# Kernel tuning notes

Hardware: AMD Instinct MI355X
Metric: run time of the kernel (lower is better)

## Reference

```python
import jax, jax.numpy as jnp
import numpy as np

NQ = 8
NL = 6
DIM = 2 ** NQ
C64 = jnp.complex64
I2 = jnp.eye(2, dtype=C64)
PX = jnp.array([[0., 1.], [1., 0.]], dtype=C64)
PY = jnp.array([[0., -1j], [1j, 0.]], dtype=C64)
PZ = jnp.array([[1., 0.], [0., -1.]], dtype=C64)
# sign of Pauli-Z eigenvalue for each computational basis state, wires 0..3 (wire 0 = MSB)
_idx = np.arange(DIM)
_SIGNS = jnp.asarray(np.stack([1.0 - 2.0 * ((_idx >> (NQ - 1 - w)) & 1) for w in range(4)]).astype(np.float32))  # (4, 256)

def _rot(t, P):
    # exp(-i t/2 P) = cos(t/2) I - i sin(t/2) P
    th = t.astype(jnp.float32) / 2
    return jnp.cos(th) * I2 - 1j * jnp.sin(th) * P

def _apply1(st, U, w):
    # apply 2x2 unitary U on wire w; st: (B, 2,2,...,2)
    s = jnp.moveaxis(st, w + 1, -1)
    return jnp.moveaxis(s @ U.T, -1, w + 1)

def _cnot(st, c, t):
    # flip target axis where control bit == 1
    s = jnp.moveaxis(st, (c + 1, t + 1), (1, 2))
    s = jnp.concatenate([s[:, :1], s[:, 1:, ::-1]], axis=1)
    return jnp.moveaxis(s, (1, 2), (c + 1, t + 1))

def _quantum(x, weights):
    B = x.shape[0]
    # AmplitudeEmbedding with normalize=True
    psi = (x / jnp.linalg.norm(x, axis=1, keepdims=True)).astype(C64)
    st = psi.reshape((B,) + (2,) * NQ)
    for l in range(NL):
        lw = weights[l]
        for q in range(NQ):
            st = _apply1(st, _rot(lw[3 * q], PX), q)
            st = _apply1(st, _rot(lw[3 * q + 1], PY), q)
            st = _apply1(st, _rot(lw[3 * q + 2], PZ), q)
        for i in range(NQ - 1):
            st = _cnot(st, i, i + 1)
        st = _cnot(st, NQ - 1, 0)
        for i in range(0, NQ, 2):
            if i + 2 < NQ:
                st = _cnot(st, i, i + 2)
    probs = jnp.abs(st.reshape(B, DIM)) ** 2
    return probs @ _SIGNS.T  # (B, 4) Z expectations on wires 0..3

def _bn(h, g, b):
    # BatchNorm1d, training mode (batch statistics, biased variance)
    m = h.mean(0)
    v = h.var(0)
    return g * (h - m) * jax.lax.rsqrt(v + 1e-5) + b

def _forward(x, q_weights, aW, ab, fW1, fb1, fW2, fb2, cW1, cb1, g1, be1, cW2, cb2, g2, be2, cW3, cb3, cW4, cb4):
    q = _quantum(x, q_weights)                     # (B, 4)
    qf = q @ aW.T + ab                             # quantum_adapter
    cf = jnp.tanh(jax.nn.relu(x @ fW1.T + fb1) @ fW2.T + fb2)  # feature_processor
    h = qf + cf
    h = jax.nn.relu(_bn(h @ cW1.T + cb1, g1, be1))
    h = jax.nn.relu(_bn(h @ cW2.T + cb2, g2, be2))
    h = jax.nn.relu(h @ cW3.T + cb3)
    return jax.nn.sigmoid(h @ cW4.T + cb4)         # (B, 1)

def setup_inputs():
    key = jax.random.key(0)
    ks = jax.random.split(key, 21)
    f32 = jnp.float32
    r = lambda k, shp, s: jax.random.normal(k, shp, dtype=f32) * s
    B = 8192
    return {
        'x': r(ks[0], (B, 256), 1.0),
        'q_weights': r(ks[1], (NL, NQ * 3), 1.0),
        'aW': r(ks[2], (4, 4), 0.5), 'ab': r(ks[3], (4,), 0.1),
        'fW1': r(ks[4], (64, 256), 0.0625), 'fb1': r(ks[5], (64,), 0.05),
        'fW2': r(ks[6], (4, 64), 0.125), 'fb2': r(ks[7], (4,), 0.05),
        'cW1': r(ks[8], (32, 4), 0.5), 'cb1': r(ks[9], (32,), 0.05),
        'g1': 1.0 + r(ks[10], (32,), 0.05), 'be1': r(ks[11], (32,), 0.05),
        'cW2': r(ks[12], (16, 32), 0.18), 'cb2': r(ks[13], (16,), 0.05),
        'g2': 1.0 + r(ks[14], (16,), 0.05), 'be2': r(ks[15], (16,), 0.05),
        'cW3': r(ks[16], (8, 16), 0.25), 'cb3': r(ks[17], (8,), 0.05),
        'cW4': r(ks[18], (1, 8), 0.35), 'cb4': r(ks[19], (1,), 0.05),
    }

def reference(x, q_weights, aW, ab, fW1, fb1, fW2, fb2, cW1, cb1, g1, be1, cW2, cb2, g2, be2, cW3, cb3, cW4, cb4):
    return _forward(x, q_weights, aW, ab, fW1, fb1, fW2, fb2, cW1, cb1, g1, be1, cW2, cb2, g2, be2, cW3, cb3, cW4, cb4)
```

## Files before the change

### kernel.cpp

```cpp
#include <hip/hip_runtime.h>
#include <math.h>

#define INV_B (1.0f / 8192.0f)

struct QTables {
    int xm[6][8];
    int rm[6][8];
    int meas[4];
};
constexpr QTables make_tables() {
    QTables T{};
    int Mrow[8] = {}, Ncol[8] = {};
    for (int b = 0; b < 8; ++b) { Mrow[b] = 1 << b; Ncol[b] = 1 << b; }
    constexpr int bc[11] = {7,6,5,4,3,2,1,0,7,5,3};
    constexpr int bt[11] = {6,5,4,3,2,1,0,7,5,3,1};
    for (int l = 0; l < 6; ++l) {
        for (int w = 0; w < 8; ++w) { T.xm[l][w] = Ncol[7 - w]; T.rm[l][w] = Mrow[7 - w]; }
        for (int k = 0; k < 11; ++k) { Mrow[bt[k]] ^= Mrow[bc[k]]; Ncol[bc[k]] ^= Ncol[bt[k]]; }
    }
    for (int w = 0; w < 4; ++w) T.meas[w] = Mrow[7 - w];
    return T;
}
constexpr QTables TB = make_tables();

template<int ML>
static __device__ __forceinline__ float lanex(float v) {
    if constexpr (ML == 0) { return v; }
    else if constexpr (ML == 1) { return __int_as_float(__builtin_amdgcn_update_dpp(0, __float_as_int(v), 0xB1, 0xF, 0xF, true)); }
    else if constexpr (ML == 2) { return __int_as_float(__builtin_amdgcn_update_dpp(0, __float_as_int(v), 0x4E, 0xF, 0xF, true)); }
    else if constexpr (ML == 3) { return __int_as_float(__builtin_amdgcn_update_dpp(0, __float_as_int(v), 0x1B, 0xF, 0xF, true)); }
    else { return __shfl_xor(v, ML, 64); }
}

static __device__ __forceinline__ float bsum64(float v) {
    v += lanex<1>(v); v += lanex<2>(v);
    v += __shfl_xor(v, 4, 64);  v += __shfl_xor(v, 8, 64);
    v += __shfl_xor(v, 16, 64); v += __shfl_xor(v, 32, 64);
    return v;
}

template<int XM, int RM>
static __device__ __forceinline__ void gate(float (&ar)[4], float (&ai)[4], const int lane,
                                            const float u00r, const float u00i,
                                            const float u01r, const float u01i) {
    constexpr int ML = XM >> 2, MR = XM & 3;
    constexpr int RL = RM >> 2, RR = RM & 3;
    const int pl = __popc(lane & RL) & 1;
    const float csi0 = pl ? -u00i : u00i;
    const float cpr0 = pl ? -u01r : u01r;
    const float csi1 = -csi0, cpr1 = -cpr0;
    float pr[4], pi[4];
    #pragma unroll
    for (int r = 0; r < 4; ++r) {
        pr[r] = lanex<ML>(ar[r ^ MR]);
        pi[r] = lanex<ML>(ai[r ^ MR]);
    }
    #pragma unroll
    for (int r = 0; r < 4; ++r) {
        const int pb = __builtin_popcount(r & RR) & 1;
        const float csi = pb ? csi1 : csi0;
        const float cpr = pb ? cpr1 : cpr0;
        const float nr = u00r * ar[r] - csi * ai[r] + cpr * pr[r] - u01i * pi[r];
        const float ni = u00r * ai[r] + csi * ar[r] + cpr * pi[r] + u01i * pr[r];
        ar[r] = nr; ai[r] = ni;
    }
}

__global__ __launch_bounds__(256) void k_pre(
        const float* __restrict__ fW1, const float* __restrict__ qw,
        float* __restrict__ U, float* __restrict__ fT, float* __restrict__ accz) {
    const int t = threadIdx.x, b = blockIdx.x;
    const int e = b * 256 + t;
    const int j = e >> 8, k = e & 255;
    fT[(k >> 2) * 256 + j * 4 + (k & 3)] = fW1[e];
    if (e < 2048) accz[e] = 0.f;
    if (b == 0 && t < 48) {
        const int l = t >> 3, q = t & 7;
        const float* a = qw + l * 24 + q * 3;
        const float h1 = 0.5f * a[0], h2 = 0.5f * a[1], h3 = 0.5f * a[2];
        const float c1 = cosf(h1), s1 = sinf(h1);
        const float c2 = cosf(h2), s2 = sinf(h2);
        const float c3 = cosf(h3), s3 = sinf(h3);
        const float m00r =  c1 * c2, m00i =  s1 * s2;
        const float m01r = -c1 * s2, m01i = -s1 * c2;
        float4 u;
        u.x = m00r * c3 + m00i * s3;  u.y = m00i * c3 - m00r * s3;
        u.z = m01r * c3 + m01i * s3;  u.w = m01i * c3 - m01r * s3;
        ((float4*)U)[t] = u;
    }
}

__global__ __launch_bounds__(256) void k_main(
        const float* __restrict__ x, const float* __restrict__ U,
        const float* __restrict__ fT,
        const float* __restrict__ fb1, const float* __restrict__ fW2,
        const float* __restrict__ fb2,
        const float* __restrict__ aW, const float* __restrict__ ab,
        float* __restrict__ hws, float* __restrict__ acc1) {
    const int t = threadIdx.x, lane = t & 63, wv = t >> 6;
    const int b = blockIdx.x;
    const int row = b * 4 + wv;

    const float4 xr = ((const float4*)(x + (long)row * 256))[lane];

    const float4* fT4 = (const float4*)fT;
    float z1 = 0.f;
    #pragma unroll 8
    for (int kk = 0; kk < 64; ++kk) {
        const float4 w4 = fT4[kk * 64 + lane];
        const float x0 = __int_as_float(__builtin_amdgcn_readlane(__float_as_int(xr.x), kk));
        const float x1 = __int_as_float(__builtin_amdgcn_readlane(__float_as_int(xr.y), kk));
        const float x2 = __int_as_float(__builtin_amdgcn_readlane(__float_as_int(xr.z), kk));
        const float x3 = __int_as_float(__builtin_amdgcn_readlane(__float_as_int(xr.w), kk));
        z1 += w4.x * x0 + w4.y * x1 + w4.z * x2 + w4.w * x3;
    }
    const float v1 = fmaxf(z1 + fb1[lane], 0.f);
    float cf[4];
    #pragma unroll
    for (int c = 0; c < 4; ++c) {
        const float s = bsum64(v1 * fW2[c * 64 + lane]);
        cf[c] = tanhf(s + fb2[c]);
    }

    float ar[4] = {xr.x, xr.y, xr.z, xr.w};
    float ai[4] = {0.f, 0.f, 0.f, 0.f};
    const float4* U4 = (const float4*)U;

#define GATE(L, W) { const float4 u = U4[(L) * 8 + (W)]; \
                     gate<TB.xm[L][W], TB.rm[L][W]>(ar, ai, lane, u.x, u.y, u.z, u.w); }
#define LAYER(L) GATE(L,0) GATE(L,1) GATE(L,2) GATE(L,3) GATE(L,4) GATE(L,5) GATE(L,6) GATE(L,7)
    LAYER(0) LAYER(1) LAYER(2) LAYER(3) LAYER(4) LAYER(5)
#undef LAYER
#undef GATE

    float pv[4];
    #pragma unroll
    for (int r = 0; r < 4; ++r) pv[r] = ar[r] * ar[r] + ai[r] * ai[r];
    float S = pv[0] + pv[1] + pv[2] + pv[3];
    float qs[4];
    #pragma unroll
    for (int w = 0; w < 4; ++w) {
        const int mm = TB.meas[w];
        const int plm = __popc(lane & (mm >> 2)) & 1;
        float s = 0.f;
        #pragma unroll
        for (int r = 0; r < 4; ++r) {
            const int sgn = plm ^ (__builtin_popcount(r & (mm & 3)) & 1);
            s += sgn ? -pv[r] : pv[r];
        }
        qs[w] = s;
    }
    S = bsum64(S);
    const float inv = 1.0f / S;
    float qe[4];
    #pragma unroll
    for (int w = 0; w < 4; ++w) qe[w] = bsum64(qs[w]) * inv;

    float h[4];
    #pragma unroll
    for (int k = 0; k < 4; ++k) {
        float s = ab[k] + cf[k];
        #pragma unroll
        for (int j = 0; j < 4; ++j) s += aW[k * 4 + j] * qe[j];
        h[k] = s;
    }
    if (lane == 0)
        ((float4*)hws)[row] = make_float4(h[0], h[1], h[2], h[3]);

    __shared__ float wsum[4][20];
    if (lane == 0) {
        #pragma unroll
        for (int k = 0; k < 4; ++k) wsum[wv][k] = h[k];
        #pragma unroll
        for (int j = 0; j < 4; ++j)
            #pragma unroll
            for (int k = 0; k < 4; ++k) wsum[wv][4 + j * 4 + k] = h[j] * h[k];
    }
    __syncthreads();
    if (t < 20)
        atomicAdd(acc1 + (b & 31) * 20 + t,
                  wsum[0][t] + wsum[1][t] + wsum[2][t] + wsum[3][t]);
}

__global__ __launch_bounds__(64) void k_mid(
        const float* __restrict__ hws, const float* __restrict__ acc1,
        const float* __restrict__ cW1, const float* __restrict__ cb1,
        const float* __restrict__ g1, const float* __restrict__ be1,
        const float* __restrict__ cW2, const float* __restrict__ cb2,
        float* __restrict__ z2ws, float* __restrict__ acc2) {
    const int t = threadIdx.x;
    __shared__ float sA[20];
    __shared__ float m1s[32], is1[32];
    if (t < 20) {
        float s = 0.f;
        for (int sl = 0; sl < 32; ++sl) s += acc1[sl * 20 + t];
        sA[t] = s;
    }
    __syncthreads();
    if (t < 32) {
        float mu[4], w[4];
        #pragma unroll
        for (int k = 0; k < 4; ++k) mu[k] = sA[k] * INV_B;
        float m = cb1[t];
        #pragma unroll
        for (int k = 0; k < 4; ++k) { w[k] = cW1[t * 4 + k]; m += w[k] * mu[k]; }
        float var = 0.f;
        #pragma unroll
        for (int a2 = 0; a2 < 4; ++a2)
            #pragma unroll
            for (int b2 = 0; b2 < 4; ++b2)
                var += w[a2] * w[b2] * (sA[4 + a2 * 4 + b2] * INV_B - mu[a2] * mu[b2]);
        m1s[t] = m;
        is1[t] = 1.0f / sqrtf(var + 1e-5f);
    }
    __syncthreads();

    const long e = (long)blockIdx.x * 64 + t;
    const float4 h4 = ((const float4*)hws)[e];
    const float h[4] = {h4.x, h4.y, h4.z, h4.w};
    float a1[32];
    #pragma unroll
    for (int j = 0; j < 32; ++j) {
        float z = cb1[j];
        #pragma unroll
        for (int k = 0; k < 4; ++k) z += cW1[j * 4 + k] * h[k];
        a1[j] = fmaxf((z - m1s[j]) * is1[j] * g1[j] + be1[j], 0.f);
    }
    float z2[16];
    #pragma unroll
    for (int k = 0; k < 16; ++k) {
        float s = cb2[k];
        #pragma unroll
        for (int j = 0; j < 32; ++j) s += cW2[k * 32 + j] * a1[j];
        z2[k] = s;
    }
    float4* zp = (float4*)(z2ws + e * 16);
    zp[0] = make_float4(z2[0], z2[1], z2[2], z2[3]);
    zp[1] = make_float4(z2[4], z2[5], z2[6], z2[7]);
    zp[2] = make_float4(z2[8], z2[9], z2[10], z2[11]);
    zp[3] = make_float4(z2[12], z2[13], z2[14], z2[15]);

    float sv[16], sq[16];
    #pragma unroll
    for (int k = 0; k < 16; ++k) { sv[k] = z2[k]; sq[k] = z2[k] * z2[k]; }
    #pragma unroll
    for (int m = 1; m < 64; m <<= 1) {
        #pragma unroll
        for (int k = 0; k < 16; ++k) {
            sv[k] += __shfl_xor(sv[k], m, 64);
            sq[k] += __shfl_xor(sq[k], m, 64);
        }
    }
    if (t == 0) {
        float* dst = acc2 + (blockIdx.x & 31) * 32;
        #pragma unroll
        for (int k = 0; k < 16; ++k) atomicAdd(dst + k, sv[k]);
        #pragma unroll
        for (int k = 0; k < 16; ++k) atomicAdd(dst + 16 + k, sq[k]);
    }
}

__global__ __launch_bounds__(64) void k_out(
        const float* __restrict__ z2ws, const float* __restrict__ acc2,
        const float* __restrict__ g2, const float* __restrict__ be2,
        const float* __restrict__ cW3, const float* __restrict__ cb3,
        const float* __restrict__ cW4, const float* __restrict__ cb4,
        float* __restrict__ out) {
    const int t = threadIdx.x;
    __shared__ float sB[32];
    __shared__ float m2s[16], is2[16];
    if (t < 32) {
        float s = 0.f;
        for (int sl = 0; sl < 32; ++sl) s += acc2[sl * 32 + t];
        sB[t] = s;
    }
    __syncthreads();
    if (t < 16) {
        const float m = sB[t] * INV_B;
        const float var = sB[16 + t] * INV_B - m * m;
        m2s[t] = m;
        is2[t] = 1.0f / sqrtf(var + 1e-5f);
    }
    __syncthreads();

    const long e = (long)blockIdx.x * 64 + t;
    const float4* zp = (const float4*)(z2ws + e * 16);
    const float4 v0 = zp[0], v1 = zp[1], v2 = zp[2], v3 = zp[3];
    const float z2[16] = {v0.x, v0.y, v0.z, v0.w, v1.x, v1.y, v1.z, v1.w,
                          v2.x, v2.y, v2.z, v2.w, v3.x, v3.y, v3.z, v3.w};
    float a2[16];
    #pragma unroll
    for (int k = 0; k < 16; ++k)
        a2[k] = fmaxf((z2[k] - m2s[k]) * is2[k] * g2[k] + be2[k], 0.f);
    float z3[8];
    #pragma unroll
    for (int j = 0; j < 8; ++j) {
        float s = cb3[j];
        #pragma unroll
        for (int k = 0; k < 16; ++k) s += cW3[j * 16 + k] * a2[k];
        z3[j] = fmaxf(s, 0.f);
    }
    float y = cb4[0];
    #pragma unroll
    for (int j = 0; j < 8; ++j) y += cW4[j] * z3[j];
    out[e] = 1.0f / (1.0f + expf(-y));
}

extern "C" void kernel_launch(void* const* d_in, const int* in_sizes, int n_in,
                              void* d_out, int out_size, void* d_ws, size_t ws_size,
                              hipStream_t stream) {
    (void)in_sizes; (void)n_in; (void)out_size; (void)ws_size;
    const float* x   = (const float*)d_in[0];
    const float* qw  = (const float*)d_in[1];
    const float* aW  = (const float*)d_in[2];
    const float* ab  = (const float*)d_in[3];
    const float* fW1 = (const float*)d_in[4];
    const float* fb1 = (const float*)d_in[5];
    const float* fW2 = (const float*)d_in[6];
    const float* fb2 = (const float*)d_in[7];
    const float* cW1 = (const float*)d_in[8];
    const float* cb1 = (const float*)d_in[9];
    const float* g1  = (const float*)d_in[10];
    const float* be1 = (const float*)d_in[11];
    const float* cW2 = (const float*)d_in[12];
    const float* cb2 = (const float*)d_in[13];
    const float* g2  = (const float*)d_in[14];
    const float* be2 = (const float*)d_in[15];
    const float* cW3 = (const float*)d_in[16];
    const float* cb3 = (const float*)d_in[17];
    const float* cW4 = (const float*)d_in[18];
    const float* cb4 = (const float*)d_in[19];

    float* ws   = (float*)d_ws;
    float* acc1 = ws;
    float* acc2 = ws + 1024;
    float* U    = ws + 2048;
    float* fT   = ws + 4096;
    float* hws  = ws + 24576;
    float* z2ws = ws + 57344;

    k_pre <<<64, 256, 0, stream>>>(fW1, qw, U, fT, ws);
    k_main<<<2048, 256, 0, stream>>>(x, U, fT, fb1, fW2, fb2, aW, ab, hws, acc1);
    k_mid <<<128, 64, 0, stream>>>(hws, acc1, cW1, cb1, g1, be1, cW2, cb2, z2ws, acc2);
    k_out <<<128, 64, 0, stream>>>(z2ws, acc2, g2, be2, cW3, cb3, cW4, cb4, (float*)d_out);
}
```

Measured before the change: 157.2 us.

## Move feature-processor GEMM to fp16 MFMA in a separate kernel

```diff
diff --git a/kernel.cpp b/kernel.cpp
--- a/kernel.cpp
+++ b/kernel.cpp
@@ -2,6 +2,10 @@
 #include <math.h>
 
 #define INV_B (1.0f / 8192.0f)
+
+typedef float  v2f  __attribute__((ext_vector_type(2)));
+typedef _Float16 half8 __attribute__((ext_vector_type(8)));
+typedef float  f32x4 __attribute__((ext_vector_type(4)));
 
 struct QTables {
     int xm[6][8];
@@ -29,18 +33,25 @@
     else if constexpr (ML == 1) { return __int_as_float(__builtin_amdgcn_update_dpp(0, __float_as_int(v), 0xB1, 0xF, 0xF, true)); }
     else if constexpr (ML == 2) { return __int_as_float(__builtin_amdgcn_update_dpp(0, __float_as_int(v), 0x4E, 0xF, 0xF, true)); }
     else if constexpr (ML == 3) { return __int_as_float(__builtin_amdgcn_update_dpp(0, __float_as_int(v), 0x1B, 0xF, 0xF, true)); }
+    else if constexpr (ML < 32) { return __int_as_float(__builtin_amdgcn_ds_swizzle(__float_as_int(v), 0x1F | (ML << 10))); }
     else { return __shfl_xor(v, ML, 64); }
 }
 
 static __device__ __forceinline__ float bsum64(float v) {
-    v += lanex<1>(v); v += lanex<2>(v);
-    v += __shfl_xor(v, 4, 64);  v += __shfl_xor(v, 8, 64);
-    v += __shfl_xor(v, 16, 64); v += __shfl_xor(v, 32, 64);
+    v += lanex<1>(v);  v += lanex<2>(v);
+    v += lanex<4>(v);  v += lanex<8>(v);
+    v += lanex<16>(v); v += __shfl_xor(v, 32, 64);
     return v;
 }
 
+static __device__ __forceinline__ float tanh_fast(float v) {
+    const float c = fminf(fmaxf(v, -10.f), 10.f);
+    const float e = __expf(2.f * c);
+    return (e - 1.f) / (e + 1.f);
+}
+
 template<int XM, int RM>
-static __device__ __forceinline__ void gate(float (&ar)[4], float (&ai)[4], const int lane,
+static __device__ __forceinline__ void gate(v2f (&z)[4], const int lane,
                                             const float u00r, const float u00i,
                                             const float u01r, const float u01i) {
     constexpr int ML = XM >> 2, MR = XM & 3;
@@ -49,31 +60,32 @@
     const float csi0 = pl ? -u00i : u00i;
     const float cpr0 = pl ? -u01r : u01r;
     const float csi1 = -csi0, cpr1 = -cpr0;
-    float pr[4], pi[4];
+    v2f p[4];
     #pragma unroll
     for (int r = 0; r < 4; ++r) {
-        pr[r] = lanex<ML>(ar[r ^ MR]);
-        pi[r] = lanex<ML>(ai[r ^ MR]);
+        p[r].x = lanex<ML>(z[r ^ MR].x);
+        p[r].y = lanex<ML>(z[r ^ MR].y);
     }
     #pragma unroll
     for (int r = 0; r < 4; ++r) {
         const int pb = __builtin_popcount(r & RR) & 1;
         const float csi = pb ? csi1 : csi0;
         const float cpr = pb ? cpr1 : cpr0;
-        const float nr = u00r * ar[r] - csi * ai[r] + cpr * pr[r] - u01i * pi[r];
-        const float ni = u00r * ai[r] + csi * ar[r] + cpr * pi[r] + u01i * pr[r];
-        ar[r] = nr; ai[r] = ni;
-    }
-}
-
-__global__ __launch_bounds__(256) void k_pre(
-        const float* __restrict__ fW1, const float* __restrict__ qw,
-        float* __restrict__ U, float* __restrict__ fT, float* __restrict__ accz) {
+        const v2f zs = { -z[r].y, z[r].x };
+        const v2f ps = { -p[r].y, p[r].x };
+        z[r] = ((u00r * z[r] + csi * zs) + cpr * p[r]) + u01i * ps;
+    }
+}
+
+#define XS 264
+__global__ __launch_bounds__(256) void k_feat(
+        const float* __restrict__ x, const float* __restrict__ qw,
+        const float* __restrict__ fW1, const float* __restrict__ fb1,
+        const float* __restrict__ fW2, const float* __restrict__ fb2,
+        float* __restrict__ U, float* __restrict__ cfws, float* __restrict__ accz) {
     const int t = threadIdx.x, b = blockIdx.x;
-    const int e = b * 256 + t;
-    const int j = e >> 8, k = e & 255;
-    fT[(k >> 2) * 256 + j * 4 + (k & 3)] = fW1[e];
-    if (e < 2048) accz[e] = 0.f;
+
+    if (t < 16) accz[b * 16 + t] = 0.f;
     if (b == 0 && t < 48) {
         const int l = t >> 3, q = t & 7;
         const float* a = qw + l * 24 + q * 3;
@@ -88,13 +100,69 @@
         u.z = m01r * c3 + m01i * s3;  u.w = m01i * c3 - m01r * s3;
         ((float4*)U)[t] = u;
     }
+
+    __shared__ _Float16 xl[64 * XS];
+    __shared__ _Float16 wl[64 * XS];
+    const long r0 = (long)b * 64;
+    #pragma unroll
+    for (int i = 0; i < 16; ++i) {
+        const int idx = i * 256 + t;
+        const int row = idx >> 6, c4 = idx & 63;
+        const float4 xv = ((const float4*)(x + (r0 + row) * 256))[c4];
+        _Float16* d = &xl[row * XS + c4 * 4];
+        d[0] = (_Float16)xv.x; d[1] = (_Float16)xv.y;
+        d[2] = (_Float16)xv.z; d[3] = (_Float16)xv.w;
+        const float4 wv = ((const float4*)(fW1 + (long)row * 256))[c4];
+        _Float16* e = &wl[row * XS + c4 * 4];
+        e[0] = (_Float16)wv.x; e[1] = (_Float16)wv.y;
+        e[2] = (_Float16)wv.z; e[3] = (_Float16)wv.w;
+    }
+    __syncthreads();
+
+    const int lane = t & 63, w4 = t >> 6;
+    const int g = lane >> 4, col = lane & 15;
+    const int rloc = w4 * 16 + col;
+
+    half8 bf[8];
+    #pragma unroll
+    for (int kb = 0; kb < 8; ++kb)
+        bf[kb] = *(const half8*)&xl[rloc * XS + kb * 32 + g * 8];
+
+    float accc[4] = {0.f, 0.f, 0.f, 0.f};
+    #pragma unroll
+    for (int jc = 0; jc < 4; ++jc) {
+        f32x4 cv = {0.f, 0.f, 0.f, 0.f};
+        #pragma unroll
+        for (int kb = 0; kb < 8; ++kb) {
+            const half8 af = *(const half8*)&wl[(jc * 16 + col) * XS + kb * 32 + g * 8];
+            cv = __builtin_amdgcn_mfma_f32_16x16x32_f16(af, bf[kb], cv, 0, 0, 0);
+        }
+        #pragma unroll
+        for (int r = 0; r < 4; ++r) {
+            const int j = jc * 16 + g * 4 + r;
+            const float z = fmaxf(cv[r] + fb1[j], 0.f);
+            #pragma unroll
+            for (int c = 0; c < 4; ++c) accc[c] += z * fW2[c * 64 + j];
+        }
+    }
+    #pragma unroll
+    for (int c = 0; c < 4; ++c) {
+        accc[c] += __shfl_xor(accc[c], 16, 64);
+        accc[c] += __shfl_xor(accc[c], 32, 64);
+    }
+    if (g == 0) {
+        float4 o;
+        o.x = tanh_fast(accc[0] + fb2[0]);
+        o.y = tanh_fast(accc[1] + fb2[1]);
+        o.z = tanh_fast(accc[2] + fb2[2]);
+        o.w = tanh_fast(accc[3] + fb2[3]);
+        ((float4*)cfws)[r0 + w4 * 16 + col] = o;
+    }
 }
 
 __global__ __launch_bounds__(256) void k_main(
         const float* __restrict__ x, const float* __restrict__ U,
-        const float* __restrict__ fT,
-        const float* __restrict__ fb1, const float* __restrict__ fW2,
-        const float* __restrict__ fb2,
+        const float* __restrict__ cfws,
         const float* __restrict__ aW, const float* __restrict__ ab,
         float* __restrict__ hws, float* __restrict__ acc1) {
     const int t = threadIdx.x, lane = t & 63, wv = t >> 6;
@@ -103,31 +171,11 @@
 
     const float4 xr = ((const float4*)(x + (long)row * 256))[lane];
 
-    const float4* fT4 = (const float4*)fT;
-    float z1 = 0.f;
-    #pragma unroll 8
-    for (int kk = 0; kk < 64; ++kk) {
-        const float4 w4 = fT4[kk * 64 + lane];
-        const float x0 = __int_as_float(__builtin_amdgcn_readlane(__float_as_int(xr.x), kk));
-        const float x1 = __int_as_float(__builtin_amdgcn_readlane(__float_as_int(xr.y), kk));
-        const float x2 = __int_as_float(__builtin_amdgcn_readlane(__float_as_int(xr.z), kk));
-        const float x3 = __int_as_float(__builtin_amdgcn_readlane(__float_as_int(xr.w), kk));
-        z1 += w4.x * x0 + w4.y * x1 + w4.z * x2 + w4.w * x3;
-    }
-    const float v1 = fmaxf(z1 + fb1[lane], 0.f);
-    float cf[4];
-    #pragma unroll
-    for (int c = 0; c < 4; ++c) {
-        const float s = bsum64(v1 * fW2[c * 64 + lane]);
-        cf[c] = tanhf(s + fb2[c]);
-    }
-
-    float ar[4] = {xr.x, xr.y, xr.z, xr.w};
-    float ai[4] = {0.f, 0.f, 0.f, 0.f};
+    v2f z[4] = { {xr.x, 0.f}, {xr.y, 0.f}, {xr.z, 0.f}, {xr.w, 0.f} };
     const float4* U4 = (const float4*)U;
 
 #define GATE(L, W) { const float4 u = U4[(L) * 8 + (W)]; \
-                     gate<TB.xm[L][W], TB.rm[L][W]>(ar, ai, lane, u.x, u.y, u.z, u.w); }
+                     gate<TB.xm[L][W], TB.rm[L][W]>(z, lane, u.x, u.y, u.z, u.w); }
 #define LAYER(L) GATE(L,0) GATE(L,1) GATE(L,2) GATE(L,3) GATE(L,4) GATE(L,5) GATE(L,6) GATE(L,7)
     LAYER(0) LAYER(1) LAYER(2) LAYER(3) LAYER(4) LAYER(5)
 #undef LAYER
@@ -135,7 +183,7 @@
 
     float pv[4];
     #pragma unroll
-    for (int r = 0; r < 4; ++r) pv[r] = ar[r] * ar[r] + ai[r] * ai[r];
+    for (int r = 0; r < 4; ++r) pv[r] = z[r].x * z[r].x + z[r].y * z[r].y;
     float S = pv[0] + pv[1] + pv[2] + pv[3];
     float qs[4];
     #pragma unroll
@@ -156,6 +204,8 @@
     #pragma unroll
     for (int w = 0; w < 4; ++w) qe[w] = bsum64(qs[w]) * inv;
 
+    const float4 cfv = ((const float4*)cfws)[row];
+    const float cf[4] = {cfv.x, cfv.y, cfv.z, cfv.w};
     float h[4];
     #pragma unroll
     for (int k = 0; k < 4; ++k) {
@@ -221,10 +271,10 @@
     float a1[32];
     #pragma unroll
     for (int j = 0; j < 32; ++j) {
-        float z = cb1[j];
-        #pragma unroll
-        for (int k = 0; k < 4; ++k) z += cW1[j * 4 + k] * h[k];
-        a1[j] = fmaxf((z - m1s[j]) * is1[j] * g1[j] + be1[j], 0.f);
+        float zz = cb1[j];
+        #pragma unroll
+        for (int k = 0; k < 4; ++k) zz += cW1[j * 4 + k] * h[k];
+        a1[j] = fmaxf((zz - m1s[j]) * is1[j] * g1[j] + be1[j], 0.f);
     }
     float z2[16];
     #pragma unroll
@@ -335,12 +385,12 @@
     float* acc1 = ws;
     float* acc2 = ws + 1024;
     float* U    = ws + 2048;
-    float* fT   = ws + 4096;
-    float* hws  = ws + 24576;
-    float* z2ws = ws + 57344;
-
-    k_pre <<<64, 256, 0, stream>>>(fW1, qw, U, fT, ws);
-    k_main<<<2048, 256, 0, stream>>>(x, U, fT, fb1, fW2, fb2, aW, ab, hws, acc1);
+    float* cfws = ws + 4096;
+    float* hws  = ws + 40960;
+    float* z2ws = ws + 81920;
+
+    k_feat<<<128, 256, 0, stream>>>(x, qw, fW1, fb1, fW2, fb2, U, cfws, ws);
+    k_main<<<2048, 256, 0, stream>>>(x, U, cfws, aW, ab, hws, acc1);
     k_mid <<<128, 64, 0, stream>>>(hws, acc1, cW1, cb1, g1, be1, cW2, cb2, z2ws, acc2);
     k_out <<<128, 64, 0, stream>>>(z2ws, acc2, g2, be2, cW3, cb3, cW4, cb4, (float*)d_out);
 }
```

Measured after the change: 148.1 us. 1.06x faster.
